# Kernel optimization log

Hardware: AMD Instinct MI355X
Metric: run time of the kernel (lower is better)

## Reference

```python
import jax, jax.numpy as jnp
import numpy as np


def setup_inputs() -> dict:
    key = jax.random.key(0)
    k1, k2 = jax.random.split(key)
    B, S, H = 64, 4096, 1024
    encoder_hidden_states = jax.random.normal(k1, (B, S, H), dtype=jnp.float32)
    decoder_hidden_state = jax.random.normal(k2, (B, H), dtype=jnp.float32)
    return {
        "encoder_hidden_states": encoder_hidden_states,
        "decoder_hidden_state": decoder_hidden_state,
    }


def reference(encoder_hidden_states, decoder_hidden_state):
    # scores: [B, S] = enc[b,s,:] . dec[b,:]
    scores = jnp.einsum("bsh,bh->bs", encoder_hidden_states, decoder_hidden_state)
    attention_weights = jax.nn.softmax(scores, axis=1)  # [B, S]
    # context: [B, H] = sum_s w[b,s] * enc[b,s,:]
    context = jnp.einsum("bsh,bs->bh", encoder_hidden_states, attention_weights)
    out = jnp.concatenate((context, decoder_hidden_state), axis=1)  # [B, 2H]
    return (out, attention_weights)
```

## Files before the change

kernel.cpp:

```cpp
#include <hip/hip_runtime.h>
#include <hip/hip_bf16.h>


#define NB 64
#define NS 4096
#define NH 1024
#define NTHREADS 256
#define NWAVES 4
#define PSTRIDE (NH + 2)

template<int NC>
__global__ __launch_bounds__(NTHREADS, 5)
void dotattn_pass_a(const float* __restrict__ enc, const float* __restrict__ dec,
                    float* __restrict__ scores, float* __restrict__ partials)
{
    const int blk   = blockIdx.x;
    const int b     = blk / NC;
    const int chunk = blk % NC;
    const int tid   = threadIdx.x;
    const int lane  = tid & 63;
    const int wave  = tid >> 6;

    const int start = (chunk * NS) / NC;
    const int end   = ((chunk + 1) * NS) / NC;

    const float* decb = dec + b * NH;
    float4 dreg[4];
#pragma unroll
    for (int k = 0; k < 4; ++k)
        dreg[k] = *reinterpret_cast<const float4*>(decb + lane * 4 + k * 256);

    float4 ctx[4];
#pragma unroll
    for (int k = 0; k < 4; ++k) ctx[k] = make_float4(0.f, 0.f, 0.f, 0.f);
    float m = -3.0e38f, l = 0.f;

    const float* encb = enc + (size_t)b * NS * NH;

    float4 en[4];
    {
        const size_t base = (size_t)(start + wave) * NH + lane * 4;
#pragma unroll
        for (int k = 0; k < 4; ++k)
            en[k] = *reinterpret_cast<const float4*>(encb + base + k * 256);
    }

    for (int s = start + wave; s < end; s += NWAVES) {
        float4 e[4];
#pragma unroll
        for (int k = 0; k < 4; ++k) e[k] = en[k];

        if (s + NWAVES < end) {
            const size_t nbase = (size_t)(s + NWAVES) * NH + lane * 4;
#pragma unroll
            for (int k = 0; k < 4; ++k)
                en[k] = *reinterpret_cast<const float4*>(encb + nbase + k * 256);
        }

        float p = 0.f;
#pragma unroll
        for (int k = 0; k < 4; ++k) {
            p += e[k].x * dreg[k].x;
            p += e[k].y * dreg[k].y;
            p += e[k].z * dreg[k].z;
            p += e[k].w * dreg[k].w;
        }
#pragma unroll
        for (int off = 32; off >= 1; off >>= 1)
            p += __shfl_xor(p, off, 64);

        if (lane == 0) scores[b * NS + s] = p;

        if (p > m) {
            const float sc = __expf(m - p);
            l *= sc;
#pragma unroll
            for (int k = 0; k < 4; ++k) {
                ctx[k].x *= sc; ctx[k].y *= sc; ctx[k].z *= sc; ctx[k].w *= sc;
            }
            m = p;
        }
        const float w = __expf(p - m);
        l += w;
#pragma unroll
        for (int k = 0; k < 4; ++k) {
            ctx[k].x += w * e[k].x; ctx[k].y += w * e[k].y;
            ctx[k].z += w * e[k].z; ctx[k].w += w * e[k].w;
        }
    }

    __shared__ float sml[NWAVES][2];
    __shared__ float sctx[NWAVES][NH];

    if (lane == 0) { sml[wave][0] = m; sml[wave][1] = l; }
    __syncthreads();

    const float M = fmaxf(fmaxf(sml[0][0], sml[1][0]), fmaxf(sml[2][0], sml[3][0]));
    float L = 0.f;
#pragma unroll
    for (int wv = 0; wv < NWAVES; ++wv)
        L += sml[wv][1] * __expf(sml[wv][0] - M);

    const float msc = __expf(m - M);
#pragma unroll
    for (int k = 0; k < 4; ++k) {
        float4 v = make_float4(ctx[k].x * msc, ctx[k].y * msc,
                               ctx[k].z * msc, ctx[k].w * msc);
        *reinterpret_cast<float4*>(&sctx[wave][lane * 4 + k * 256]) = v;
    }
    __syncthreads();

    float* outp = partials + (size_t)(b * NC + chunk) * PSTRIDE;
    for (int h = tid; h < NH; h += NTHREADS)
        outp[h] = sctx[0][h] + sctx[1][h] + sctx[2][h] + sctx[3][h];
    if (tid == 0) { outp[NH] = M; outp[NH + 1] = L; }
}

template<int NC>
__global__ __launch_bounds__(NTHREADS)
void dotattn_finalize(const float* __restrict__ dec, const float* __restrict__ scores,
                      const float* __restrict__ partials, float* __restrict__ out)
{
    const int b   = blockIdx.x >> 2;
    const int q   = blockIdx.x & 3;
    const int tid = threadIdx.x;
    const float* pb = partials + (size_t)b * NC * PSTRIDE;

    float M = -3.0e38f;
#pragma unroll
    for (int c = 0; c < NC; ++c)
        M = fmaxf(M, pb[c * PSTRIDE + NH]);

    float scale[NC];
    float L = 0.f;
#pragma unroll
    for (int c = 0; c < NC; ++c) {
        scale[c] = __expf(pb[c * PSTRIDE + NH] - M);
        L += pb[c * PSTRIDE + NH + 1] * scale[c];
    }
    const float invL = 1.0f / L;

    {
        const int h = q * 256 + tid;
        float acc = 0.f;
#pragma unroll
        for (int c = 0; c < NC; ++c)
            acc += pb[c * PSTRIDE + h] * scale[c];
        float* ob = out + (size_t)b * 2 * NH;
        ob[h]      = acc * invL;
        ob[NH + h] = dec[b * NH + h];
    }

    const float* sc = scores + (size_t)b * NS + q * 1024;
    float* wb = out + (size_t)NB * 2 * NH + (size_t)b * NS + q * 1024;
    for (int s = tid; s < 1024; s += NTHREADS)
        wb[s] = __expf(sc[s] - M) * invL;
}

extern "C" void kernel_launch(void* const* d_in, const int* in_sizes, int n_in,
                              void* d_out, int out_size, void* d_ws, size_t ws_size,
                              hipStream_t stream)
{
    const float* enc;
    const float* dec;
    if (in_sizes[0] == NB * NH) {
        dec = (const float*)d_in[0];
        enc = (const float*)d_in[1];
    } else {
        enc = (const float*)d_in[0];
        dec = (const float*)d_in[1];
    }
    float* out = (float*)d_out;

    float* scores   = (float*)d_ws;
    float* partials = scores + (size_t)NB * NS;

    const size_t need20 = (size_t)NB * NS * 4 + (size_t)NB * 20 * PSTRIDE * 4;
    if (ws_size >= need20) {
        dotattn_pass_a<20><<<NB * 20, NTHREADS, 0, stream>>>(enc, dec, scores, partials);
        dotattn_finalize<20><<<NB * 4, NTHREADS, 0, stream>>>(dec, scores, partials, out);
    } else {
        dotattn_pass_a<16><<<NB * 16, NTHREADS, 0, stream>>>(enc, dec, scores, partials);
        dotattn_finalize<16><<<NB * 4, NTHREADS, 0, stream>>>(dec, scores, partials, out);
    }
}
```

Measured before the change: 206.2 us.

## Fuse finalize into main pass via last-block atomic counter, use nontemporal loads

Replaces the two-kernel scheme with a single fused kernel. In it, the last block per batch, found with an atomic counter after a threadfence, performs the cross-chunk softmax merge and writes the context and weights. Encoder loads now use nontemporal hints, the chunk count drops from 20 to 16, and the launch-bounds occupancy hint is removed. This removes a kernel launch and the gap between kernels, but adds a memset launch, a serial tail in which one block per batch writes 4096 weights, and fewer blocks in flight.

```diff
diff --git a/kernel.cpp b/kernel.cpp
--- a/kernel.cpp
+++ b/kernel.cpp
@@ -5,118 +5,234 @@
 #define NB 64
 #define NS 4096
 #define NH 1024
+#define NC 16
 #define NTHREADS 256
 #define NWAVES 4
+#define ROWS (NS / NC)
 #define PSTRIDE (NH + 2)
 
-template<int NC>
-__global__ __launch_bounds__(NTHREADS, 5)
+typedef float f32x4 __attribute__((ext_vector_type(4)));
+
+__device__ __forceinline__ f32x4 nt_load4(const float* p) {
+    return __builtin_nontemporal_load(reinterpret_cast<const f32x4*>(p));
+}
+
+__global__ __launch_bounds__(NTHREADS)
+void dotattn_fused(const float* __restrict__ enc, const float* __restrict__ dec,
+                   float* __restrict__ scores, float* __restrict__ partials,
+                   int* __restrict__ counters, float* __restrict__ out)
+{
+    const int blk   = blockIdx.x;
+    const int b     = blk >> 4;
+    const int chunk = blk & (NC - 1);
+    const int tid   = threadIdx.x;
+    const int lane  = tid & 63;
+    const int wave  = tid >> 6;
+
+    const float* decb = dec + b * NH;
+    f32x4 dreg[4];
+#pragma unroll
+    for (int k = 0; k < 4; ++k)
+        dreg[k] = *reinterpret_cast<const f32x4*>(decb + lane * 4 + k * 256);
+
+    f32x4 ctx[4];
+#pragma unroll
+    for (int k = 0; k < 4; ++k) ctx[k] = (f32x4){0.f, 0.f, 0.f, 0.f};
+    float m = -3.0e38f, l = 0.f;
+
+    const int start = chunk * ROWS;
+    const float* encb = enc + (size_t)b * NS * NH;
+
+    f32x4 en[4];
+    {
+        const size_t base = (size_t)(start + wave) * NH + lane * 4;
+#pragma unroll
+        for (int k = 0; k < 4; ++k)
+            en[k] = nt_load4(encb + base + k * 256);
+    }
+
+    for (int s = start + wave; s < start + ROWS; s += NWAVES) {
+        f32x4 e[4];
+#pragma unroll
+        for (int k = 0; k < 4; ++k) e[k] = en[k];
+
+        if (s + NWAVES < start + ROWS) {
+            const size_t nbase = (size_t)(s + NWAVES) * NH + lane * 4;
+#pragma unroll
+            for (int k = 0; k < 4; ++k)
+                en[k] = nt_load4(encb + nbase + k * 256);
+        }
+
+        f32x4 p4 = e[0] * dreg[0];
+#pragma unroll
+        for (int k = 1; k < 4; ++k) p4 += e[k] * dreg[k];
+        float p = p4.x + p4.y + p4.z + p4.w;
+#pragma unroll
+        for (int off = 32; off >= 1; off >>= 1)
+            p += __shfl_xor(p, off, 64);
+
+        if (lane == 0) scores[b * NS + s] = p;
+
+        if (p > m) {
+            const float sc = __expf(m - p);
+            l *= sc;
+#pragma unroll
+            for (int k = 0; k < 4; ++k) ctx[k] *= sc;
+            m = p;
+        }
+        const float w = __expf(p - m);
+        l += w;
+#pragma unroll
+        for (int k = 0; k < 4; ++k) ctx[k] += w * e[k];
+    }
+
+    __shared__ float sml[NWAVES][2];
+    __shared__ float sctx[NWAVES][NH];
+
+    if (lane == 0) { sml[wave][0] = m; sml[wave][1] = l; }
+    __syncthreads();
+
+    const float M = fmaxf(fmaxf(sml[0][0], sml[1][0]), fmaxf(sml[2][0], sml[3][0]));
+    float L = 0.f;
+#pragma unroll
+    for (int wv = 0; wv < NWAVES; ++wv)
+        L += sml[wv][1] * __expf(sml[wv][0] - M);
+
+    const float msc = __expf(m - M);
+#pragma unroll
+    for (int k = 0; k < 4; ++k) {
+        f32x4 v = ctx[k] * msc;
+        *reinterpret_cast<f32x4*>(&sctx[wave][lane * 4 + k * 256]) = v;
+    }
+    __syncthreads();
+
+    float* outp = partials + (size_t)(b * NC + chunk) * PSTRIDE;
+    for (int h = tid; h < NH; h += NTHREADS)
+        outp[h] = sctx[0][h] + sctx[1][h] + sctx[2][h] + sctx[3][h];
+    if (tid == 0) { outp[NH] = M; outp[NH + 1] = L; }
+
+    __threadfence();
+    __syncthreads();
+    __shared__ int s_last;
+    if (tid == 0)
+        s_last = (atomicAdd(&counters[b], 1) == NC - 1) ? 1 : 0;
+    __syncthreads();
+    if (!s_last) return;
+    __threadfence();
+
+    const float* pb = partials + (size_t)b * NC * PSTRIDE;
+    float Mg = -3.0e38f;
+#pragma unroll
+    for (int c = 0; c < NC; ++c)
+        Mg = fmaxf(Mg, pb[c * PSTRIDE + NH]);
+
+    float scale[NC];
+    float Lg = 0.f;
+#pragma unroll
+    for (int c = 0; c < NC; ++c) {
+        scale[c] = __expf(pb[c * PSTRIDE + NH] - Mg);
+        Lg += pb[c * PSTRIDE + NH + 1] * scale[c];
+    }
+    const float invL = 1.0f / Lg;
+
+    float* ob = out + (size_t)b * 2 * NH;
+    for (int h = tid; h < NH; h += NTHREADS) {
+        float acc = 0.f;
+#pragma unroll
+        for (int c = 0; c < NC; ++c)
+            acc += pb[c * PSTRIDE + h] * scale[c];
+        ob[h]      = acc * invL;
+        ob[NH + h] = decb[h];
+    }
+
+    float* wb = out + (size_t)NB * 2 * NH + (size_t)b * NS;
+    const float* sc = scores + (size_t)b * NS;
+    for (int s = tid; s < NS; s += NTHREADS)
+        wb[s] = __expf(sc[s] - Mg) * invL;
+}
+
+__global__ __launch_bounds__(NTHREADS)
 void dotattn_pass_a(const float* __restrict__ enc, const float* __restrict__ dec,
                     float* __restrict__ scores, float* __restrict__ partials)
 {
     const int blk   = blockIdx.x;
-    const int b     = blk / NC;
-    const int chunk = blk % NC;
+    const int b     = blk >> 4;
+    const int chunk = blk & (NC - 1);
     const int tid   = threadIdx.x;
     const int lane  = tid & 63;
     const int wave  = tid >> 6;
 
-    const int start = (chunk * NS) / NC;
-    const int end   = ((chunk + 1) * NS) / NC;
-
     const float* decb = dec + b * NH;
-    float4 dreg[4];
+    f32x4 dreg[4];
 #pragma unroll
     for (int k = 0; k < 4; ++k)
-        dreg[k] = *reinterpret_cast<const float4*>(decb + lane * 4 + k * 256);
-
-    float4 ctx[4];
-#pragma unroll
-    for (int k = 0; k < 4; ++k) ctx[k] = make_float4(0.f, 0.f, 0.f, 0.f);
+        dreg[k] = *reinterpret_cast<const f32x4*>(decb + lane * 4 + k * 256);
+
+    f32x4 ctx[4];
+#pragma unroll
+    for (int k = 0; k < 4; ++k) ctx[k] = (f32x4){0.f, 0.f, 0.f, 0.f};
     float m = -3.0e38f, l = 0.f;
 
+    const int start = chunk * ROWS;
     const float* encb = enc + (size_t)b * NS * NH;
 
-    float4 en[4];
+    f32x4 en[4];
     {
         const size_t base = (size_t)(start + wave) * NH + lane * 4;
 #pragma unroll
-        for (int k = 0; k < 4; ++k)
-            en[k] = *reinterpret_cast<const float4*>(encb + base + k * 256);
-    }
-
-    for (int s = start + wave; s < end; s += NWAVES) {
-        float4 e[4];
+        for (int k = 0; k < 4; ++k) en[k] = nt_load4(encb + base + k * 256);
+    }
+
+    for (int s = start + wave; s < start + ROWS; s += NWAVES) {
+        f32x4 e[4];
 #pragma unroll
         for (int k = 0; k < 4; ++k) e[k] = en[k];
-
-        if (s + NWAVES < end) {
+        if (s + NWAVES < start + ROWS) {
             const size_t nbase = (size_t)(s + NWAVES) * NH + lane * 4;
 #pragma unroll
-            for (int k = 0; k < 4; ++k)
-                en[k] = *reinterpret_cast<const float4*>(encb + nbase + k * 256);
+            for (int k = 0; k < 4; ++k) en[k] = nt_load4(encb + nbase + k * 256);
         }
-
-        float p = 0.f;
-#pragma unroll
-        for (int k = 0; k < 4; ++k) {
-            p += e[k].x * dreg[k].x;
-            p += e[k].y * dreg[k].y;
-            p += e[k].z * dreg[k].z;
-            p += e[k].w * dreg[k].w;
-        }
-#pragma unroll
-        for (int off = 32; off >= 1; off >>= 1)
-            p += __shfl_xor(p, off, 64);
-
+        f32x4 p4 = e[0] * dreg[0];
+#pragma unroll
+        for (int k = 1; k < 4; ++k) p4 += e[k] * dreg[k];
+        float p = p4.x + p4.y + p4.z + p4.w;
+#pragma unroll
+        for (int off = 32; off >= 1; off >>= 1) p += __shfl_xor(p, off, 64);
         if (lane == 0) scores[b * NS + s] = p;
-
         if (p > m) {
             const float sc = __expf(m - p);
             l *= sc;
 #pragma unroll
-            for (int k = 0; k < 4; ++k) {
-                ctx[k].x *= sc; ctx[k].y *= sc; ctx[k].z *= sc; ctx[k].w *= sc;
-            }
+            for (int k = 0; k < 4; ++k) ctx[k] *= sc;
             m = p;
         }
         const float w = __expf(p - m);
         l += w;
 #pragma unroll
-        for (int k = 0; k < 4; ++k) {
-            ctx[k].x += w * e[k].x; ctx[k].y += w * e[k].y;
-            ctx[k].z += w * e[k].z; ctx[k].w += w * e[k].w;
-        }
+        for (int k = 0; k < 4; ++k) ctx[k] += w * e[k];
     }
 
     __shared__ float sml[NWAVES][2];
     __shared__ float sctx[NWAVES][NH];
-
     if (lane == 0) { sml[wave][0] = m; sml[wave][1] = l; }
     __syncthreads();
-
     const float M = fmaxf(fmaxf(sml[0][0], sml[1][0]), fmaxf(sml[2][0], sml[3][0]));
     float L = 0.f;
 #pragma unroll
-    for (int wv = 0; wv < NWAVES; ++wv)
-        L += sml[wv][1] * __expf(sml[wv][0] - M);
-
+    for (int wv = 0; wv < NWAVES; ++wv) L += sml[wv][1] * __expf(sml[wv][0] - M);
     const float msc = __expf(m - M);
 #pragma unroll
     for (int k = 0; k < 4; ++k) {
-        float4 v = make_float4(ctx[k].x * msc, ctx[k].y * msc,
-                               ctx[k].z * msc, ctx[k].w * msc);
-        *reinterpret_cast<float4*>(&sctx[wave][lane * 4 + k * 256]) = v;
-    }
-    __syncthreads();
-
+        f32x4 v = ctx[k] * msc;
+        *reinterpret_cast<f32x4*>(&sctx[wave][lane * 4 + k * 256]) = v;
+    }
+    __syncthreads();
     float* outp = partials + (size_t)(b * NC + chunk) * PSTRIDE;
     for (int h = tid; h < NH; h += NTHREADS)
         outp[h] = sctx[0][h] + sctx[1][h] + sctx[2][h] + sctx[3][h];
     if (tid == 0) { outp[NH] = M; outp[NH + 1] = L; }
 }
 
-template<int NC>
 __global__ __launch_bounds__(NTHREADS)
 void dotattn_finalize(const float* __restrict__ dec, const float* __restrict__ scores,
                       const float* __restrict__ partials, float* __restrict__ out)
@@ -128,9 +244,7 @@
 
     float M = -3.0e38f;
 #pragma unroll
-    for (int c = 0; c < NC; ++c)
-        M = fmaxf(M, pb[c * PSTRIDE + NH]);
-
+    for (int c = 0; c < NC; ++c) M = fmaxf(M, pb[c * PSTRIDE + NH]);
     float scale[NC];
     float L = 0.f;
 #pragma unroll
@@ -144,13 +258,11 @@
         const int h = q * 256 + tid;
         float acc = 0.f;
 #pragma unroll
-        for (int c = 0; c < NC; ++c)
-            acc += pb[c * PSTRIDE + h] * scale[c];
+        for (int c = 0; c < NC; ++c) acc += pb[c * PSTRIDE + h] * scale[c];
         float* ob = out + (size_t)b * 2 * NH;
         ob[h]      = acc * invL;
         ob[NH + h] = dec[b * NH + h];
     }
-
     const float* sc = scores + (size_t)b * NS + q * 1024;
     float* wb = out + (size_t)NB * 2 * NH + (size_t)b * NS + q * 1024;
     for (int s = tid; s < 1024; s += NTHREADS)
@@ -172,15 +284,21 @@
     }
     float* out = (float*)d_out;
 
-    float* scores   = (float*)d_ws;
-    float* partials = scores + (size_t)NB * NS;
-
-    const size_t need20 = (size_t)NB * NS * 4 + (size_t)NB * 20 * PSTRIDE * 4;
-    if (ws_size >= need20) {
-        dotattn_pass_a<20><<<NB * 20, NTHREADS, 0, stream>>>(enc, dec, scores, partials);
-        dotattn_finalize<20><<<NB * 4, NTHREADS, 0, stream>>>(dec, scores, partials, out);
+    const size_t cnt_bytes   = 256;
+    const size_t score_bytes = (size_t)NB * NS * 4;
+    const size_t part_bytes  = (size_t)NB * NC * PSTRIDE * 4;
+    int*   counters = (int*)d_ws;
+    float* scores   = (float*)((char*)d_ws + cnt_bytes);
+    float* partials = (float*)((char*)d_ws + cnt_bytes + score_bytes);
+
+    if (ws_size >= cnt_bytes + score_bytes + part_bytes) {
+        hipMemsetAsync(counters, 0, cnt_bytes, stream);
+        dotattn_fused<<<NB * NC, NTHREADS, 0, stream>>>(enc, dec, scores, partials,
+                                                        counters, out);
     } else {
-        dotattn_pass_a<16><<<NB * 16, NTHREADS, 0, stream>>>(enc, dec, scores, partials);
-        dotattn_finalize<16><<<NB * 4, NTHREADS, 0, stream>>>(dec, scores, partials, out);
-    }
-}
+        float* scores2   = (float*)d_ws;
+        float* partials2 = scores2 + (size_t)NB * NS;
+        dotattn_pass_a<<<NB * NC, NTHREADS, 0, stream>>>(enc, dec, scores2, partials2);
+        dotattn_finalize<<<NB * 4, NTHREADS, 0, stream>>>(dec, scores2, partials2, out);
+    }
+}
```

New measurement: 361.7 us. 75.4% more time.
